# Optimization experiments

Hardware: AMD Instinct MI355X
Metric: run time of the kernel (lower is better)

## Reference

```python
import jax, jax.numpy as jnp
import numpy as np

POS_SIZE = 63
LATENT_SIZE = 256
NUM_CLUSTERS = 64
N = 524288


def setup_inputs() -> dict:
    key = jax.random.key(0)
    k1, k2, k3, k4 = jax.random.split(key, 4)
    X = jax.random.normal(k1, (N, POS_SIZE + LATENT_SIZE), dtype=jnp.float32)
    cluster_ids = jax.random.randint(k2, (N,), 0, NUM_CLUSTERS, dtype=jnp.int32)
    # nn.Linear weights have shape [out_features, in_features]
    W_pos = jax.random.normal(k3, (3 * NUM_CLUSTERS, POS_SIZE), dtype=jnp.float32) * 0.1
    W_feat = jax.random.normal(k4, (3 * NUM_CLUSTERS, LATENT_SIZE), dtype=jnp.float32) * 0.1
    return {"X": X, "cluster_ids": cluster_ids, "W_pos": W_pos, "W_feat": W_feat}


def reference(X, cluster_ids, W_pos, W_feat):
    # Dense projections: [N, 3*num_clusters]
    rgb_clusters = (
        jnp.einsum("np,cp->nc", X[:, :POS_SIZE], W_pos)
        + jnp.einsum("nl,cl->nc", X[:, POS_SIZE:], W_feat)
    )
    # Per-row gather of the 3 columns belonging to this row's cluster.
    cols = 3 * cluster_ids[:, None] + jnp.arange(3, dtype=cluster_ids.dtype)[None, :]  # [N, 3]
    rgb = jnp.take_along_axis(rgb_clusters, cols, axis=1)  # [N, 3]
    return rgb
```

## Files before the change

### kernel.cpp

```cpp
#include <hip/hip_runtime.h>


constexpr int POS = 63, LAT = 256, DIM = 319, NCH = 192;
constexpr int ROWS = 32;
constexpr int KPAD = 328;
constexpr int CST  = 196;
constexpr int PW_DW = NCH * 160;
constexpr size_t PW_BYTES = (size_t)PW_DW * 4;
constexpr int TILE_F4 = ROWS * DIM / 4;
constexpr int TPB = 4;

typedef __attribute__((ext_vector_type(8))) short short8;
typedef __attribute__((ext_vector_type(4))) float f32x4;

__device__ __forceinline__ unsigned f2bf(float f) {
    unsigned u = __float_as_uint(f);
    return (u + 0x7fffu + ((u >> 16) & 1u)) >> 16;
}

__global__ __launch_bounds__(256) void pack_weights(
    const float* __restrict__ Wp, const float* __restrict__ Wf,
    unsigned* __restrict__ pw)
{
    const int idx = blockIdx.x * 256 + threadIdx.x;
    if (idx >= PW_DW) return;
    const int ch = idx / 160, d = idx - ch * 160;
    auto wat = [&](int k) -> float {
        if (k < POS) return Wp[ch * POS + k];
        if (k < DIM) return Wf[ch * LAT + (k - POS)];
        return 0.f;
    };
    pw[idx] = f2bf(wat(2 * d)) | (f2bf(wat(2 * d + 1)) << 16);
}

__global__ __launch_bounds__(256, 2) void lad_mfma(
    const float4* __restrict__ X4, const int* __restrict__ cid,
    const unsigned* __restrict__ pw, float* __restrict__ out,
    int ntiles, long nf4)
{
    __shared__ __align__(16) unsigned short xb[ROWS * KPAD];
    __shared__ float cbuf[ROWS * CST];

    const int thr = threadIdx.x;
    const int l   = thr & 63;
    const int wid = thr >> 6;
    const int n0  = wid * 48;
    const int cl  = l & 15;
    const int q   = l >> 4;

    short8 Bf[3][10];
#pragma unroll
    for (int nt = 0; nt < 3; ++nt)
#pragma unroll
        for (int kk = 0; kk < 10; ++kk) {
            const unsigned* p = pw + (size_t)(n0 + nt * 16 + cl) * 160
                                   + kk * 16 + q * 4;
            Bf[nt][kk] = *reinterpret_cast<const short8*>(p);
        }

    if (thr < ROWS) xb[thr * KPAD + 319] = 0;

    const int t0 = blockIdx.x * TPB;
    const int tend = min(t0 + TPB, ntiles);
    if (t0 >= tend) return;

    float4 xr[10];
    {
        const long b4 = (long)t0 * TILE_F4;
#pragma unroll
        for (int i = 0; i < 10; ++i) {
            long idx = b4 + i * 256 + thr;
            if (idx >= nf4) idx = nf4 - 1;
            xr[i] = X4[idx];
        }
    }

    for (int t = t0; t < tend; ++t) {
        if (t > t0 && thr < 96) {
            const int r = thr / 3, j = thr - r * 3;
            const int c = cid[(size_t)(t - 1) * ROWS + r];
            out[((size_t)(t - 1) * ROWS + r) * 3 + j] = cbuf[r * CST + 3 * c + j];
        }

        {
#pragma unroll
            for (int i = 0; i < 10; ++i) {
                const int s = i * 256 + thr;
                const float4 v = xr[i];
#pragma unroll
                for (int e = 0; e < 4; ++e) {
                    const int p = 4 * s + e;
                    const float f = (e == 0) ? v.x : (e == 1) ? v.y
                                  : (e == 2) ? v.z : v.w;
                    const int r = (int)((unsigned)p / 319u);
                    if (r < ROWS) {
                        const int k = p - r * 319;
                        xb[r * KPAD + k] = (unsigned short)f2bf(f);
                    }
                }
            }
        }

        if (t + 1 < tend) {
            const long b4 = (long)(t + 1) * TILE_F4;
#pragma unroll
            for (int i = 0; i < 10; ++i) {
                long idx = b4 + i * 256 + thr;
                if (idx >= nf4) idx = nf4 - 1;
                xr[i] = X4[idx];
            }
        }

        __syncthreads();

        f32x4 acc[2][3];
#pragma unroll
        for (int mt = 0; mt < 2; ++mt)
#pragma unroll
            for (int nt = 0; nt < 3; ++nt)
                acc[mt][nt] = (f32x4)0.0f;

#pragma unroll
        for (int kk = 0; kk < 10; ++kk) {
            short8 Af[2];
#pragma unroll
            for (int mt = 0; mt < 2; ++mt) {
                const int row = mt * 16 + cl;
                const int k   = kk * 32 + q * 8;
                Af[mt] = *reinterpret_cast<const short8*>(&xb[row * KPAD + k]);
            }
#pragma unroll
            for (int mt = 0; mt < 2; ++mt)
#pragma unroll
                for (int nt = 0; nt < 3; ++nt)
                    acc[mt][nt] = __builtin_amdgcn_mfma_f32_16x16x32_bf16(
                        Af[mt], Bf[nt][kk], acc[mt][nt], 0, 0, 0);
        }

#pragma unroll
        for (int mt = 0; mt < 2; ++mt)
#pragma unroll
            for (int nt = 0; nt < 3; ++nt)
#pragma unroll
                for (int j = 0; j < 4; ++j) {
                    const int row = mt * 16 + q * 4 + j;
                    const int col = n0 + nt * 16 + cl;
                    cbuf[row * CST + col] = acc[mt][nt][j];
                }

        __syncthreads();
    }

    if (thr < 96) {
        const int t = tend - 1;
        const int r = thr / 3, j = thr - r * 3;
        const int c = cid[(size_t)t * ROWS + r];
        out[((size_t)t * ROWS + r) * 3 + j] = cbuf[r * CST + 3 * c + j];
    }
}

template <int CTRL>
__device__ __forceinline__ float dpp_add_step(float x) {
    int s = __builtin_amdgcn_update_dpp(0, __float_as_int(x), CTRL,
                                        0xF, 0xF, true);
    return x + __int_as_float(s);
}
__device__ __forceinline__ float wave_reduce_sum(float x) {
    x = dpp_add_step<0x111>(x);
    x = dpp_add_step<0x112>(x);
    x = dpp_add_step<0x114>(x);
    x = dpp_add_step<0x118>(x);
    x = dpp_add_step<0x142>(x);
    x = dpp_add_step<0x143>(x);
    return x;
}

__global__ __launch_bounds__(256) void lad_fallback(
    const float* __restrict__ X, const int* __restrict__ cid,
    const float* __restrict__ Wp, const float* __restrict__ Wf,
    float* __restrict__ out, int n)
{
    const int lane = threadIdx.x & 63;
    const int wave = (int)((blockIdx.x * blockDim.x + threadIdx.x) >> 6);
    if (wave >= n) return;
    const size_t row = (size_t)wave;
    const float* xrow = X + row * (size_t)DIM;
    const float* xf   = xrow + POS;
    const int c3 = cid[row] * 3;
    const float* wp0 = Wp + (size_t)c3 * POS;
    const float* wf0 = Wf + (size_t)c3 * LAT;
    float a0 = 0.f, a1 = 0.f, a2 = 0.f;
#pragma unroll
    for (int i = 0; i < 4; ++i) {
        const int k = lane + 64 * i;
        const float x = xf[k];
        a0 = fmaf(x, wf0[k], a0);
        a1 = fmaf(x, wf0[k + LAT], a1);
        a2 = fmaf(x, wf0[k + 2 * LAT], a2);
    }
    if (lane < POS) {
        const float x = xrow[lane];
        a0 = fmaf(x, wp0[lane], a0);
        a1 = fmaf(x, wp0[lane + POS], a1);
        a2 = fmaf(x, wp0[lane + 2 * POS], a2);
    }
    a0 = wave_reduce_sum(a0);
    a1 = wave_reduce_sum(a1);
    a2 = wave_reduce_sum(a2);
    if (lane == 63) {
        float* o = out + row * 3;
        o[0] = a0; o[1] = a1; o[2] = a2;
    }
}

extern "C" void kernel_launch(void* const* d_in, const int* in_sizes, int n_in,
                              void* d_out, int out_size, void* d_ws, size_t ws_size,
                              hipStream_t stream) {
    const float* X   = (const float*)d_in[0];
    const int*   cid = (const int*)d_in[1];
    const float* Wp  = (const float*)d_in[2];
    const float* Wf  = (const float*)d_in[3];
    float* out = (float*)d_out;
    const int n = in_sizes[1];

    if (ws_size >= PW_BYTES && n > 0 && (n % ROWS) == 0) {
        unsigned* pw = (unsigned*)d_ws;
        pack_weights<<<(PW_DW + 255) / 256, 256, 0, stream>>>(Wp, Wf, pw);
        const int ntiles = n / ROWS;
        const int grid = (ntiles + TPB - 1) / TPB;
        const long nf4 = (long)n * DIM / 4;
        lad_mfma<<<grid, 256, 0, stream>>>((const float4*)X, cid, pw, out,
                                           ntiles, nf4);
    } else {
        const int blocks = (n + 3) / 4;
        lad_fallback<<<blocks, 256, 0, stream>>>(X, cid, Wp, Wf, out, n);
    }
}
```

Baseline: 165.7 us.

## Stage X tiles directly into LDS with async loads and convert at fragment read

Replaces the register-staged fp32-to-bf16 conversion scatter with `global_load_lds` copies that move raw fp32 tiles straight into a double-buffered shared array. Conversion to bf16 now happens when MFMA A fragments are read, using packed `v_cvt_pk_bf16_f32`. The epilogue drops the shared result buffer and writes each row's three selected channels straight from the accumulators, using cluster ids loaded up front. Tiles per block go from 4 to 16. The double fp32 buffer takes about 80 KB of LDS, which likely limits the CU to one block. The fragment reads are unvectorised and use an odd row stride, and the last row can read one element past the buffer, which only the zero-padded weight cancels.

Measured after the change: 153.9 us. -7.1%, faster.

```diff
diff --git a/kernel.cpp b/kernel.cpp
--- a/kernel.cpp
+++ b/kernel.cpp
@@ -3,12 +3,11 @@
 
 constexpr int POS = 63, LAT = 256, DIM = 319, NCH = 192;
 constexpr int ROWS = 32;
-constexpr int KPAD = 328;
-constexpr int CST  = 196;
 constexpr int PW_DW = NCH * 160;
 constexpr size_t PW_BYTES = (size_t)PW_DW * 4;
-constexpr int TILE_F4 = ROWS * DIM / 4;
-constexpr int TPB = 4;
+constexpr int TILE_DW = ROWS * DIM;
+constexpr int TILE_F4 = TILE_DW / 4;
+constexpr int TPB = 16;
 
 typedef __attribute__((ext_vector_type(8))) short short8;
 typedef __attribute__((ext_vector_type(4))) float f32x4;
@@ -33,13 +32,12 @@
     pw[idx] = f2bf(wat(2 * d)) | (f2bf(wat(2 * d + 1)) << 16);
 }
 
-__global__ __launch_bounds__(256, 2) void lad_mfma(
+__global__ __launch_bounds__(256, 2) void lad_mfma2(
     const float4* __restrict__ X4, const int* __restrict__ cid,
     const unsigned* __restrict__ pw, float* __restrict__ out,
-    int ntiles, long nf4)
+    int ntiles)
 {
-    __shared__ __align__(16) unsigned short xb[ROWS * KPAD];
-    __shared__ float cbuf[ROWS * CST];
+    __shared__ float xb[2][TILE_DW];
 
     const int thr = threadIdx.x;
     const int l   = thr & 63;
@@ -52,66 +50,40 @@
 #pragma unroll
     for (int nt = 0; nt < 3; ++nt)
 #pragma unroll
-        for (int kk = 0; kk < 10; ++kk) {
-            const unsigned* p = pw + (size_t)(n0 + nt * 16 + cl) * 160
-                                   + kk * 16 + q * 4;
-            Bf[nt][kk] = *reinterpret_cast<const short8*>(p);
-        }
-
-    if (thr < ROWS) xb[thr * KPAD + 319] = 0;
+        for (int kk = 0; kk < 10; ++kk)
+            Bf[nt][kk] = *reinterpret_cast<const short8*>(
+                pw + (size_t)(n0 + nt * 16 + cl) * 160 + kk * 16 + q * 4);
 
     const int t0 = blockIdx.x * TPB;
     const int tend = min(t0 + TPB, ntiles);
     if (t0 >= tend) return;
 
-    float4 xr[10];
-    {
-        const long b4 = (long)t0 * TILE_F4;
-#pragma unroll
-        for (int i = 0; i < 10; ++i) {
-            long idx = b4 + i * 256 + thr;
-            if (idx >= nf4) idx = nf4 - 1;
-            xr[i] = X4[idx];
+    auto stage = [&](int tile, int p) {
+        const float4* src = X4 + (size_t)tile * TILE_F4;
+#pragma unroll
+        for (int j = 0; j < 10; ++j) {
+            const int slot = j * 256 + thr;
+            if (slot < TILE_F4)
+                __builtin_amdgcn_global_load_lds(
+                    (const __attribute__((address_space(1))) unsigned int*)(src + slot),
+                    (__attribute__((address_space(3))) unsigned int*)&xb[p][slot * 4],
+                    16, 0, 0);
         }
-    }
-
+    };
+
+    stage(t0, 0);
+    __syncthreads();
+
+    int p = 0;
     for (int t = t0; t < tend; ++t) {
-        if (t > t0 && thr < 96) {
-            const int r = thr / 3, j = thr - r * 3;
-            const int c = cid[(size_t)(t - 1) * ROWS + r];
-            out[((size_t)(t - 1) * ROWS + r) * 3 + j] = cbuf[r * CST + 3 * c + j];
-        }
-
-        {
-#pragma unroll
-            for (int i = 0; i < 10; ++i) {
-                const int s = i * 256 + thr;
-                const float4 v = xr[i];
-#pragma unroll
-                for (int e = 0; e < 4; ++e) {
-                    const int p = 4 * s + e;
-                    const float f = (e == 0) ? v.x : (e == 1) ? v.y
-                                  : (e == 2) ? v.z : v.w;
-                    const int r = (int)((unsigned)p / 319u);
-                    if (r < ROWS) {
-                        const int k = p - r * 319;
-                        xb[r * KPAD + k] = (unsigned short)f2bf(f);
-                    }
-                }
-            }
-        }
-
-        if (t + 1 < tend) {
-            const long b4 = (long)(t + 1) * TILE_F4;
-#pragma unroll
-            for (int i = 0; i < 10; ++i) {
-                long idx = b4 + i * 256 + thr;
-                if (idx >= nf4) idx = nf4 - 1;
-                xr[i] = X4[idx];
-            }
-        }
-
-        __syncthreads();
+        if (t + 1 < tend) stage(t + 1, p ^ 1);
+
+        int c3v[2][4];
+#pragma unroll
+        for (int mt = 0; mt < 2; ++mt)
+#pragma unroll
+            for (int j = 0; j < 4; ++j)
+                c3v[mt][j] = 3 * cid[(size_t)t * ROWS + mt * 16 + q * 4 + j];
 
         f32x4 acc[2][3];
 #pragma unroll
@@ -125,9 +97,14 @@
             short8 Af[2];
 #pragma unroll
             for (int mt = 0; mt < 2; ++mt) {
-                const int row = mt * 16 + cl;
-                const int k   = kk * 32 + q * 8;
-                Af[mt] = *reinterpret_cast<const short8*>(&xb[row * KPAD + k]);
+                const float* fp = &xb[p][(mt * 16 + cl) * DIM + kk * 32 + q * 8];
+                union { unsigned u[4]; short8 s; } cv;
+#pragma unroll
+                for (int h = 0; h < 4; ++h) {
+                    asm("v_cvt_pk_bf16_f32 %0, %1, %2"
+                        : "=v"(cv.u[h]) : "v"(fp[2 * h]), "v"(fp[2 * h + 1]));
+                }
+                Af[mt] = cv.s;
             }
 #pragma unroll
             for (int mt = 0; mt < 2; ++mt)
@@ -140,22 +117,20 @@
 #pragma unroll
         for (int mt = 0; mt < 2; ++mt)
 #pragma unroll
-            for (int nt = 0; nt < 3; ++nt)
-#pragma unroll
-                for (int j = 0; j < 4; ++j) {
-                    const int row = mt * 16 + q * 4 + j;
+            for (int j = 0; j < 4; ++j) {
+                const int grow = t * ROWS + mt * 16 + q * 4 + j;
+                const int c3 = c3v[mt][j];
+#pragma unroll
+                for (int nt = 0; nt < 3; ++nt) {
                     const int col = n0 + nt * 16 + cl;
-                    cbuf[row * CST + col] = acc[mt][nt][j];
+                    const unsigned d = (unsigned)(col - c3);
+                    if (d < 3u)
+                        out[(size_t)grow * 3 + d] = acc[mt][nt][j];
                 }
+            }
 
         __syncthreads();
-    }
-
-    if (thr < 96) {
-        const int t = tend - 1;
-        const int r = thr / 3, j = thr - r * 3;
-        const int c = cid[(size_t)t * ROWS + r];
-        out[((size_t)t * ROWS + r) * 3 + j] = cbuf[r * CST + 3 * c + j];
+        p ^= 1;
     }
 }
 
@@ -228,9 +203,8 @@
         pack_weights<<<(PW_DW + 255) / 256, 256, 0, stream>>>(Wp, Wf, pw);
         const int ntiles = n / ROWS;
         const int grid = (ntiles + TPB - 1) / TPB;
-        const long nf4 = (long)n * DIM / 4;
-        lad_mfma<<<grid, 256, 0, stream>>>((const float4*)X, cid, pw, out,
-                                           ntiles, nf4);
+        lad_mfma2<<<grid, 256, 0, stream>>>((const float4*)X, cid, pw, out,
+                                            ntiles);
     } else {
         const int blocks = (n + 3) / 4;
         lad_fallback<<<blocks, 256, 0, stream>>>(X, cid, Wp, Wf, out, n);
```
